# Kernel optimization log

Measured on AMD Instinct MI355X. Metric: run time of the kernel, lower is better.

## Reference

```python
import jax, jax.numpy as jnp
import numpy as np

WINDOW_SIZE = 512
CAUSAL = True

def _sliding_window_mask(seq_len, window_size, causal):
    i = jnp.arange(seq_len)[:, None]
    j = jnp.arange(seq_len)[None, :]
    mask = (j >= i - window_size + 1) & (j <= i)
    if causal:
        mask = mask & (j <= i)
    return mask  # [S, S] bool, True = attend


def setup_inputs() -> dict:
    key = jax.random.key(0)
    k1, k2, k3 = jax.random.split(key, 3)
    B, S, D = 16, 4096, 64
    q = jax.random.normal(k1, (B, S, D), dtype=jnp.float32)
    k = jax.random.normal(k2, (B, S, D), dtype=jnp.float32)
    v = jax.random.normal(k3, (B, S, D), dtype=jnp.float32)
    return {"q": q, "k": k, "v": v}


def reference(q, k, v):
    B, S, D = q.shape
    scale = D ** -0.5
    mask = _sliding_window_mask(S, WINDOW_SIZE, CAUSAL)  # [S, S]
    scores = jnp.einsum("bqd,bkd->bqk", q, k) * scale    # [B, S, S]
    mask_value = -jnp.finfo(scores.dtype).max
    scores = jnp.where(mask[None, :, :], scores, mask_value)
    attn = jax.nn.softmax(scores, axis=-1)
    out = jnp.einsum("bqk,bkd->bqd", attn, v)            # [B, S, D]
    return out
```

## Files before the change

kernel.cpp:

```cpp
#include <hip/hip_runtime.h>

#define BATCH 16
#define SEQ   4096
#define DIM   64
#define WIN   512

constexpr int BM = 128;
constexpr int BN = 64;
constexpr int NTHREADS = 512;
constexpr int KS = DIM + 8;
constexpr int VS = BN + 4;
constexpr int OS = DIM + 4;
constexpr int KBYTES   = BN * KS * 2;
constexpr int VBYTES   = DIM * VS * 2;
constexpr int BUFBYTES = KBYTES + VBYTES;
constexpr int SMEMBYTES = 2 * BUFBYTES;

constexpr float QSCALE  = 0.125f * 1.44269504088896340736f;
constexpr float MASKVAL = -3.0e38f;
constexpr float DEFER_THR = 8.0f;

typedef _Float16 f16x2 __attribute__((ext_vector_type(2)));
typedef _Float16 f16x4 __attribute__((ext_vector_type(4)));
typedef _Float16 f16x8 __attribute__((ext_vector_type(8)));
typedef float    f32x4 __attribute__((ext_vector_type(4)));

__device__ __forceinline__ f16x2 pk2(float a, float b) {
    return __builtin_bit_cast(f16x2, __builtin_amdgcn_cvt_pkrtz(a, b));
}

__device__ __forceinline__ void stage_kv2(_Float16* __restrict__ Ksh, _Float16* __restrict__ Vsh,
                                          const float4& k0, const float4& k1,
                                          const float4& v0, const float4& v1,
                                          int row2, int c4) {
    union { f16x4 v; f16x2 h[2]; } uk;
    uk.h[0] = pk2(k0.x, k0.y);
    uk.h[1] = pk2(k0.z, k0.w);
    *(f16x4*)&Ksh[(row2 + 0) * KS + c4] = uk.v;
    uk.h[0] = pk2(k1.x, k1.y);
    uk.h[1] = pk2(k1.z, k1.w);
    *(f16x4*)&Ksh[(row2 + 1) * KS + c4] = uk.v;
    *(f16x2*)&Vsh[(c4 + 0) * VS + row2] = pk2(v0.x, v1.x);
    *(f16x2*)&Vsh[(c4 + 1) * VS + row2] = pk2(v0.y, v1.y);
    *(f16x2*)&Vsh[(c4 + 2) * VS + row2] = pk2(v0.z, v1.z);
    *(f16x2*)&Vsh[(c4 + 3) * VS + row2] = pk2(v0.w, v1.w);
}

__global__ __launch_bounds__(NTHREADS, 4)
void swa_kernel(const float* __restrict__ qg, const float* __restrict__ kg,
                const float* __restrict__ vg, float* __restrict__ outg) {
    __shared__ __align__(16) char smem[SMEMBYTES];
    float* Osh = (float*)smem;

    const int tid  = threadIdx.x;
    const int lane = tid & 63;
    const int wave = tid >> 6;
    const int lr   = lane & 15;
    const int quad = lane >> 4;

    static_assert(SEQ / BM == 32 && BATCH == 16, "swizzle assumes 512 blocks");
    const int lin    = blockIdx.x + (SEQ / BM) * blockIdx.y;
    const int xcd    = lin & 7;
    const int slot   = lin >> 3;
    const int member = slot & 3;
    const int gchunk = (slot >> 2) * 8 + xcd;
    const int b      = gchunk >> 3;
    const int qblk   = (gchunk & 7) * 4 + member;

    const int qrow0 = qblk * BM;
    const int wr0   = qrow0 + wave * 16;
    const int q     = wr0 + lr;

    const float* qb = qg + (size_t)b * SEQ * DIM;
    const float* kb = kg + (size_t)b * SEQ * DIM;
    const float* vb = vg + (size_t)b * SEQ * DIM;
    float*       ob = outg + (size_t)b * SEQ * DIM;

    const int row2 = (tid >> 4) * 2;
    const int c4   = (tid & 15) * 4;

    const float* qp = qb + (size_t)q * DIM + quad * 8;
    const float4 a0 = *(const float4*)(qp + 0);
    const float4 a1 = *(const float4*)(qp + 4);
    const float4 a2 = *(const float4*)(qp + 32);
    const float4 a3 = *(const float4*)(qp + 36);
    union { f16x8 v; f16x2 h[4]; } uq0, uq1;
    uq0.h[0] = pk2(a0.x * QSCALE, a0.y * QSCALE);
    uq0.h[1] = pk2(a0.z * QSCALE, a0.w * QSCALE);
    uq0.h[2] = pk2(a1.x * QSCALE, a1.y * QSCALE);
    uq0.h[3] = pk2(a1.z * QSCALE, a1.w * QSCALE);
    uq1.h[0] = pk2(a2.x * QSCALE, a2.y * QSCALE);
    uq1.h[1] = pk2(a2.z * QSCALE, a2.w * QSCALE);
    uq1.h[2] = pk2(a3.x * QSCALE, a3.y * QSCALE);
    uq1.h[3] = pk2(a3.z * QSCALE, a3.w * QSCALE);
    const f16x8 qf0 = uq0.v, qf1 = uq1.v;

    f32x4 o[4];
    #pragma unroll
    for (int mi = 0; mi < 4; ++mi) o[mi] = (f32x4){0.f, 0.f, 0.f, 0.f};
    float m_run = -1e30f, l_run = 0.f;

    const int t0 = (qrow0 > (WIN - 1)) ? (qrow0 - (WIN - 1)) >> 6 : 0;
    const int t1 = (qrow0 + BM - 1) >> 6;

    {
        const size_t g0 = (size_t)(t0 * BN + row2) * DIM + c4;
        const float4 k0 = *(const float4*)&kb[g0];
        const float4 v0 = *(const float4*)&vb[g0];
        const float4 k1 = *(const float4*)&kb[g0 + DIM];
        const float4 v1 = *(const float4*)&vb[g0 + DIM];
        stage_kv2((_Float16*)smem, (_Float16*)(smem + KBYTES), k0, k1, v0, v1, row2, c4);
    }
    __syncthreads();

    for (int t = t0; t <= t1; ++t) {
        const int cb = (t - t0) & 1;
        const _Float16* Kc = (const _Float16*)(smem + cb * BUFBYTES);
        const _Float16* Vc = (const _Float16*)(smem + cb * BUFBYTES + KBYTES);
        const bool have_next = (t < t1);

        float4 kp0, kp1, vp0, vp1;
        if (have_next) {
            const size_t g0 = (size_t)((t + 1) * BN + row2) * DIM + c4;
            kp0 = *(const float4*)&kb[g0];
            vp0 = *(const float4*)&vb[g0];
            kp1 = *(const float4*)&kb[g0 + DIM];
            vp1 = *(const float4*)&vb[g0 + DIM];
        }

        const int kbase = t * BN;
        const bool active = (kbase + BN - 1 >= wr0 - (WIN - 1)) && (kbase <= wr0 + 15);
        if (active) {
            f32x4 sc[4];
            #pragma unroll
            for (int mt = 0; mt < 4; ++mt) {
                const f16x8 kf0 = *(const f16x8*)&Kc[(mt * 16 + lr) * KS + quad * 8];
                const f16x8 kf1 = *(const f16x8*)&Kc[(mt * 16 + lr) * KS + 32 + quad * 8];
                f32x4 s = (f32x4){0.f, 0.f, 0.f, 0.f};
                s = __builtin_amdgcn_mfma_f32_16x16x32_f16(kf0, qf0, s, 0, 0, 0);
                s = __builtin_amdgcn_mfma_f32_16x16x32_f16(kf1, qf1, s, 0, 0, 0);
                sc[mt] = s;
            }

            const bool edge = (kbase < wr0 + 15 - (WIN - 1)) || (kbase + BN - 1 > wr0);
            if (edge) {
                #pragma unroll
                for (int mt = 0; mt < 4; ++mt) {
                    #pragma unroll
                    for (int r = 0; r < 4; ++r) {
                        const int key = kbase + mt * 16 + quad * 4 + r;
                        sc[mt][r] = ((unsigned)(q - key) < (unsigned)WIN) ? sc[mt][r] : MASKVAL;
                    }
                }
            }

            const float pmA = fmaxf(fmaxf(sc[0][0], sc[0][1]), fmaxf(sc[0][2], sc[0][3]));
            const float pmB = fmaxf(fmaxf(sc[1][0], sc[1][1]), fmaxf(sc[1][2], sc[1][3]));
            const float pmC = fmaxf(fmaxf(sc[2][0], sc[2][1]), fmaxf(sc[2][2], sc[2][3]));
            const float pmD = fmaxf(fmaxf(sc[3][0], sc[3][1]), fmaxf(sc[3][2], sc[3][3]));
            float pm = fmaxf(fmaxf(pmA, pmB), fmaxf(pmC, pmD));
            pm = fmaxf(pm, __shfl_xor(pm, 16));
            pm = fmaxf(pm, __shfl_xor(pm, 32));

            if (__any(pm > m_run + DEFER_THR)) {
                const float mn    = fmaxf(m_run, pm);
                const float alpha = exp2f(m_run - mn);
                m_run = mn;
                l_run *= alpha;
                #pragma unroll
                for (int mi = 0; mi < 4; ++mi) o[mi] = o[mi] * alpha;
            }

            f16x4 pb[4];
            float ls = 0.f;
            #pragma unroll
            for (int nt = 0; nt < 4; ++nt) {
                const float p0 = exp2f(sc[nt][0] - m_run);
                const float p1 = exp2f(sc[nt][1] - m_run);
                const float p2 = exp2f(sc[nt][2] - m_run);
                const float p3 = exp2f(sc[nt][3] - m_run);
                ls += (p0 + p1) + (p2 + p3);
                union { f16x4 v; f16x2 h[2]; } up;
                up.h[0] = pk2(p0, p1);
                up.h[1] = pk2(p2, p3);
                pb[nt] = up.v;
            }
            l_run += ls;

            #pragma unroll
            for (int nt = 0; nt < 4; ++nt) {
                #pragma unroll
                for (int mi = 0; mi < 4; ++mi) {
                    const f16x4 vf = *(const f16x4*)&Vc[(mi * 16 + lr) * VS + nt * 16 + quad * 4];
                    o[mi] = __builtin_amdgcn_mfma_f32_16x16x16f16(vf, pb[nt], o[mi], 0, 0, 0);
                }
            }
        }

        if (have_next) {
            _Float16* Kn = (_Float16*)(smem + (cb ^ 1) * BUFBYTES);
            _Float16* Vn = (_Float16*)(smem + (cb ^ 1) * BUFBYTES + KBYTES);
            stage_kv2(Kn, Vn, kp0, kp1, vp0, vp1, row2, c4);
        }
        __syncthreads();
    }

    l_run += __shfl_xor(l_run, 16);
    l_run += __shfl_xor(l_run, 32);
    const float inv = 1.0f / l_run;

    float* Ow = Osh + wave * 16 * OS;
    #pragma unroll
    for (int mi = 0; mi < 4; ++mi) {
        float4 st;
        st.x = o[mi][0] * inv; st.y = o[mi][1] * inv;
        st.z = o[mi][2] * inv; st.w = o[mi][3] * inv;
        *(float4*)&Ow[lr * OS + mi * 16 + quad * 4] = st;
    }
    #pragma unroll
    for (int j = 0; j < 4; ++j) {
        const int qq = quad + 4 * j;
        const int d4 = lr * 4;
        const float4 vst = *(const float4*)&Ow[qq * OS + d4];
        *(float4*)&ob[(size_t)(wr0 + qq) * DIM + d4] = vst;
    }
}

extern "C" void kernel_launch(void* const* d_in, const int* in_sizes, int n_in,
                              void* d_out, int out_size, void* d_ws, size_t ws_size,
                              hipStream_t stream) {
    (void)in_sizes; (void)n_in; (void)out_size; (void)d_ws; (void)ws_size;
    const float* q = (const float*)d_in[0];
    const float* k = (const float*)d_in[1];
    const float* v = (const float*)d_in[2];
    float* out = (float*)d_out;
    dim3 grid(SEQ / BM, BATCH);
    swa_kernel<<<grid, dim3(NTHREADS), 0, stream>>>(q, k, v, out);
}
```

Before: 107.3 us.

## Halve query block to 64 rows and skip fully masked 16-key subtiles per wave

Reduces the query tile from 128 to 64 rows with 256 threads, so each thread stages four K/V rows per tile, and adjusts the XCD swizzle for 1024 blocks. Inside each key tile, every wave computes the range of 16-key subtiles that intersect its window and skips the QK MFMAs, masking, exp and PV MFMAs for subtiles outside it, replacing the old all-or-nothing active check. A sched_barrier is placed after the prefetch loads. Smaller blocks cut the number of wasted key tiles per block, at the cost of re-reading K/V across more blocks and more per-subtile branching.

```diff
diff --git a/kernel.cpp b/kernel.cpp
--- a/kernel.cpp
+++ b/kernel.cpp
@@ -5,9 +5,9 @@
 #define DIM   64
 #define WIN   512
 
-constexpr int BM = 128;
+constexpr int BM = 64;
 constexpr int BN = 64;
-constexpr int NTHREADS = 512;
+constexpr int NTHREADS = 256;
 constexpr int KS = DIM + 8;
 constexpr int VS = BN + 4;
 constexpr int OS = DIM + 4;
@@ -29,21 +29,48 @@
     return __builtin_bit_cast(f16x2, __builtin_amdgcn_cvt_pkrtz(a, b));
 }
 
-__device__ __forceinline__ void stage_kv2(_Float16* __restrict__ Ksh, _Float16* __restrict__ Vsh,
-                                          const float4& k0, const float4& k1,
-                                          const float4& v0, const float4& v1,
-                                          int row2, int c4) {
-    union { f16x4 v; f16x2 h[2]; } uk;
-    uk.h[0] = pk2(k0.x, k0.y);
-    uk.h[1] = pk2(k0.z, k0.w);
-    *(f16x4*)&Ksh[(row2 + 0) * KS + c4] = uk.v;
-    uk.h[0] = pk2(k1.x, k1.y);
-    uk.h[1] = pk2(k1.z, k1.w);
-    *(f16x4*)&Ksh[(row2 + 1) * KS + c4] = uk.v;
-    *(f16x2*)&Vsh[(c4 + 0) * VS + row2] = pk2(v0.x, v1.x);
-    *(f16x2*)&Vsh[(c4 + 1) * VS + row2] = pk2(v0.y, v1.y);
-    *(f16x2*)&Vsh[(c4 + 2) * VS + row2] = pk2(v0.z, v1.z);
-    *(f16x2*)&Vsh[(c4 + 3) * VS + row2] = pk2(v0.w, v1.w);
+struct Pref {
+    float4 k0, k1, k2, k3;
+    float4 v0, v1, v2, v3;
+};
+
+__device__ __forceinline__ void load_tile(Pref& p, const float* __restrict__ kb,
+                                          const float* __restrict__ vb,
+                                          int kbase, int row4, int c4) {
+    const size_t g = (size_t)(kbase + row4) * DIM + c4;
+    p.k0 = *(const float4*)&kb[g + 0 * DIM];
+    p.k1 = *(const float4*)&kb[g + 1 * DIM];
+    p.k2 = *(const float4*)&kb[g + 2 * DIM];
+    p.k3 = *(const float4*)&kb[g + 3 * DIM];
+    p.v0 = *(const float4*)&vb[g + 0 * DIM];
+    p.v1 = *(const float4*)&vb[g + 1 * DIM];
+    p.v2 = *(const float4*)&vb[g + 2 * DIM];
+    p.v3 = *(const float4*)&vb[g + 3 * DIM];
+}
+
+__device__ __forceinline__ void stage_tile(char* __restrict__ buf, const Pref& p,
+                                           int row4, int c4) {
+    _Float16* Ksh = (_Float16*)buf;
+    _Float16* Vsh = (_Float16*)(buf + KBYTES);
+    union { f16x4 v; f16x2 h[2]; } u;
+    u.h[0] = pk2(p.k0.x, p.k0.y); u.h[1] = pk2(p.k0.z, p.k0.w);
+    *(f16x4*)&Ksh[(row4 + 0) * KS + c4] = u.v;
+    u.h[0] = pk2(p.k1.x, p.k1.y); u.h[1] = pk2(p.k1.z, p.k1.w);
+    *(f16x4*)&Ksh[(row4 + 1) * KS + c4] = u.v;
+    u.h[0] = pk2(p.k2.x, p.k2.y); u.h[1] = pk2(p.k2.z, p.k2.w);
+    *(f16x4*)&Ksh[(row4 + 2) * KS + c4] = u.v;
+    u.h[0] = pk2(p.k3.x, p.k3.y); u.h[1] = pk2(p.k3.z, p.k3.w);
+    *(f16x4*)&Ksh[(row4 + 3) * KS + c4] = u.v;
+    const float* f0 = (const float*)&p.v0;
+    const float* f1 = (const float*)&p.v1;
+    const float* f2 = (const float*)&p.v2;
+    const float* f3 = (const float*)&p.v3;
+    #pragma unroll
+    for (int j = 0; j < 4; ++j) {
+        u.h[0] = pk2(f0[j], f1[j]);
+        u.h[1] = pk2(f2[j], f3[j]);
+        *(f16x4*)&Vsh[(c4 + j) * VS + row4] = u.v;
+    }
 }
 
 __global__ __launch_bounds__(NTHREADS, 4)
@@ -58,14 +85,14 @@
     const int lr   = lane & 15;
     const int quad = lane >> 4;
 
-    static_assert(SEQ / BM == 32 && BATCH == 16, "swizzle assumes 512 blocks");
+    static_assert(SEQ / BM == 64 && BATCH == 16, "swizzle assumes 1024 blocks");
     const int lin    = blockIdx.x + (SEQ / BM) * blockIdx.y;
     const int xcd    = lin & 7;
     const int slot   = lin >> 3;
-    const int member = slot & 3;
-    const int gchunk = (slot >> 2) * 8 + xcd;
+    const int member = slot & 7;
+    const int gchunk = (slot >> 3) * 8 + xcd;
     const int b      = gchunk >> 3;
-    const int qblk   = (gchunk & 7) * 4 + member;
+    const int qblk   = (gchunk & 7) * 8 + member;
 
     const int qrow0 = qblk * BM;
     const int wr0   = qrow0 + wave * 16;
@@ -76,7 +103,7 @@
     const float* vb = vg + (size_t)b * SEQ * DIM;
     float*       ob = outg + (size_t)b * SEQ * DIM;
 
-    const int row2 = (tid >> 4) * 2;
+    const int row4 = (tid >> 4) * 4;
     const int c4   = (tid & 15) * 4;
 
     const float* qp = qb + (size_t)q * DIM + quad * 8;
@@ -103,14 +130,9 @@
     const int t0 = (qrow0 > (WIN - 1)) ? (qrow0 - (WIN - 1)) >> 6 : 0;
     const int t1 = (qrow0 + BM - 1) >> 6;
 
-    {
-        const size_t g0 = (size_t)(t0 * BN + row2) * DIM + c4;
-        const float4 k0 = *(const float4*)&kb[g0];
-        const float4 v0 = *(const float4*)&vb[g0];
-        const float4 k1 = *(const float4*)&kb[g0 + DIM];
-        const float4 v1 = *(const float4*)&vb[g0 + DIM];
-        stage_kv2((_Float16*)smem, (_Float16*)(smem + KBYTES), k0, k1, v0, v1, row2, c4);
-    }
+    Pref pf;
+    load_tile(pf, kb, vb, t0 * BN, row4, c4);
+    stage_tile(smem, pf, row4, c4);
     __syncthreads();
 
     for (int t = t0; t <= t1; ++t) {
@@ -119,21 +141,18 @@
         const _Float16* Vc = (const _Float16*)(smem + cb * BUFBYTES + KBYTES);
         const bool have_next = (t < t1);
 
-        float4 kp0, kp1, vp0, vp1;
-        if (have_next) {
-            const size_t g0 = (size_t)((t + 1) * BN + row2) * DIM + c4;
-            kp0 = *(const float4*)&kb[g0];
-            vp0 = *(const float4*)&vb[g0];
-            kp1 = *(const float4*)&kb[g0 + DIM];
-            vp1 = *(const float4*)&vb[g0 + DIM];
-        }
+        if (have_next) load_tile(pf, kb, vb, (t + 1) * BN, row4, c4);
+        __builtin_amdgcn_sched_barrier(0);
 
         const int kbase = t * BN;
-        const bool active = (kbase + BN - 1 >= wr0 - (WIN - 1)) && (kbase <= wr0 + 15);
-        if (active) {
-            f32x4 sc[4];
-            #pragma unroll
-            for (int mt = 0; mt < 4; ++mt) {
+        const int u    = (wr0 - kbase) >> 4;
+        const int mtlo = (u - 32 > 0) ? u - 32 : 0;
+        const int mthi = (u < 3) ? u : 3;
+
+        f32x4 sc[4];
+        #pragma unroll
+        for (int mt = 0; mt < 4; ++mt) {
+            if (mt >= mtlo && mt <= mthi) {
                 const f16x8 kf0 = *(const f16x8*)&Kc[(mt * 16 + lr) * KS + quad * 8];
                 const f16x8 kf1 = *(const f16x8*)&Kc[(mt * 16 + lr) * KS + 32 + quad * 8];
                 f32x4 s = (f32x4){0.f, 0.f, 0.f, 0.f};
@@ -141,11 +160,14 @@
                 s = __builtin_amdgcn_mfma_f32_16x16x32_f16(kf1, qf1, s, 0, 0, 0);
                 sc[mt] = s;
             }
-
-            const bool edge = (kbase < wr0 + 15 - (WIN - 1)) || (kbase + BN - 1 > wr0);
-            if (edge) {
-                #pragma unroll
-                for (int mt = 0; mt < 4; ++mt) {
+        }
+
+        const bool edge = (kbase + mtlo * 16 < wr0 + 15 - (WIN - 1)) ||
+                          (kbase + mthi * 16 + 15 > wr0);
+        if (edge) {
+            #pragma unroll
+            for (int mt = 0; mt < 4; ++mt) {
+                if (mt >= mtlo && mt <= mthi) {
                     #pragma unroll
                     for (int r = 0; r < 4; ++r) {
                         const int key = kbase + mt * 16 + quad * 4 + r;
@@ -153,28 +175,33 @@
                     }
                 }
             }
-
-            const float pmA = fmaxf(fmaxf(sc[0][0], sc[0][1]), fmaxf(sc[0][2], sc[0][3]));
-            const float pmB = fmaxf(fmaxf(sc[1][0], sc[1][1]), fmaxf(sc[1][2], sc[1][3]));
-            const float pmC = fmaxf(fmaxf(sc[2][0], sc[2][1]), fmaxf(sc[2][2], sc[2][3]));
-            const float pmD = fmaxf(fmaxf(sc[3][0], sc[3][1]), fmaxf(sc[3][2], sc[3][3]));
-            float pm = fmaxf(fmaxf(pmA, pmB), fmaxf(pmC, pmD));
-            pm = fmaxf(pm, __shfl_xor(pm, 16));
-            pm = fmaxf(pm, __shfl_xor(pm, 32));
-
-            if (__any(pm > m_run + DEFER_THR)) {
-                const float mn    = fmaxf(m_run, pm);
-                const float alpha = exp2f(m_run - mn);
-                m_run = mn;
-                l_run *= alpha;
-                #pragma unroll
-                for (int mi = 0; mi < 4; ++mi) o[mi] = o[mi] * alpha;
-            }
-
-            f16x4 pb[4];
-            float ls = 0.f;
+        }
+
+        float pm = MASKVAL;
+        #pragma unroll
+        for (int mt = 0; mt < 4; ++mt) {
+            if (mt >= mtlo && mt <= mthi) {
+                pm = fmaxf(pm, fmaxf(fmaxf(sc[mt][0], sc[mt][1]),
+                                     fmaxf(sc[mt][2], sc[mt][3])));
+            }
+        }
+        pm = fmaxf(pm, __shfl_xor(pm, 16));
+        pm = fmaxf(pm, __shfl_xor(pm, 32));
+
+        if (__any(pm > m_run + DEFER_THR)) {
+            const float mn    = fmaxf(m_run, pm);
+            const float alpha = exp2f(m_run - mn);
+            m_run = mn;
+            l_run *= alpha;
             #pragma unroll
-            for (int nt = 0; nt < 4; ++nt) {
+            for (int mi = 0; mi < 4; ++mi) o[mi] = o[mi] * alpha;
+        }
+
+        f16x4 pb[4];
+        float ls = 0.f;
+        #pragma unroll
+        for (int nt = 0; nt < 4; ++nt) {
+            if (nt >= mtlo && nt <= mthi) {
                 const float p0 = exp2f(sc[nt][0] - m_run);
                 const float p1 = exp2f(sc[nt][1] - m_run);
                 const float p2 = exp2f(sc[nt][2] - m_run);
@@ -185,10 +212,12 @@
                 up.h[1] = pk2(p2, p3);
                 pb[nt] = up.v;
             }
-            l_run += ls;
-
-            #pragma unroll
-            for (int nt = 0; nt < 4; ++nt) {
+        }
+        l_run += ls;
+
+        #pragma unroll
+        for (int nt = 0; nt < 4; ++nt) {
+            if (nt >= mtlo && nt <= mthi) {
                 #pragma unroll
                 for (int mi = 0; mi < 4; ++mi) {
                     const f16x4 vf = *(const f16x4*)&Vc[(mi * 16 + lr) * VS + nt * 16 + quad * 4];
@@ -197,11 +226,7 @@
             }
         }
 
-        if (have_next) {
-            _Float16* Kn = (_Float16*)(smem + (cb ^ 1) * BUFBYTES);
-            _Float16* Vn = (_Float16*)(smem + (cb ^ 1) * BUFBYTES + KBYTES);
-            stage_kv2(Kn, Vn, kp0, kp1, vp0, vp1, row2, c4);
-        }
+        if (have_next) stage_tile(smem + (cb ^ 1) * BUFBYTES, pf, row4, c4);
         __syncthreads();
     }
 
```

New measurement: 116.1 us. 1.08x slower.
